# Kernel tuning notes

Measured on AMD Instinct MI355X. Metric: run time of the kernel, lower is better.

## Reference

```python
import jax, jax.numpy as jnp
import numpy as np

# Geometry constants (equidistant flat-detector fan beam)
B, A, D = 16, 1024, 1024      # batch, n_projections, detector bins
H, W = 512, 512               # reconstruction grid
VX = 1.0                      # pixel spacing (mm)
DU = 1.25                     # detector bin spacing (mm)
D_SI = 750.0                  # source-isocenter distance (mm)
D_SD = 1200.0                 # source-detector distance (mm)


def setup_inputs() -> dict:
    key = jax.random.key(0)
    sino = jax.random.normal(key, (B, A, D), dtype=jnp.float32)
    # Ram-Lak ramp filter in FFT ordering (matches torch.fft.fft bin layout)
    filt = jnp.asarray(np.abs(np.fft.fftfreq(D)).astype(np.float32))
    angles = jnp.asarray(np.linspace(0.0, 2.0 * np.pi, A, endpoint=False).astype(np.float32))
    return {"sinogram": sino, "filt": filt, "angles": angles}


def _backproject(fsino, angles):
    # fsino: [B, A, D] filtered sinogram -> image [B, H, W]
    xs = (jnp.arange(W, dtype=jnp.float32) - (W - 1) / 2.0) * VX
    ys = (jnp.arange(H, dtype=jnp.float32) - (H - 1) / 2.0) * VX
    X, Y = jnp.meshgrid(xs, ys, indexing="xy")  # [H, W] world coords (mm)

    def body(acc, inp):
        beta, proj = inp  # beta scalar, proj [B, D]
        c, s = jnp.cos(beta), jnp.sin(beta)
        t = D_SI + X * c + Y * s            # distance from source along central ray [H,W]
        u = D_SD * (-X * s + Y * c) / t     # detector coordinate (mm) [H,W]
        idx = u / DU + (D - 1) / 2.0        # fractional detector index
        i0 = jnp.clip(jnp.floor(idx), 0, D - 2).astype(jnp.int32)
        frac = jnp.clip(idx - i0.astype(jnp.float32), 0.0, 1.0)
        inside = (idx >= 0.0) & (idx <= D - 1.0)
        v0 = jnp.take(proj, i0, axis=1)       # [B, H, W]
        v1 = jnp.take(proj, i0 + 1, axis=1)   # [B, H, W]
        val = v0 * (1.0 - frac) + v1 * frac
        w = (D_SI / t) ** 2                   # fan-beam distance weighting
        acc = acc + jnp.where(inside, val * w, 0.0)
        return acc, None

    acc0 = jnp.zeros((B, H, W), jnp.float32)
    acc, _ = jax.lax.scan(body, acc0, (angles, jnp.swapaxes(fsino, 0, 1)))
    return acc * (jnp.pi / A)  # angular integration step


def reference(sinogram, filt, angles):
    # FFT ramp filtering along detector axis (ortho norm, as in torch code)
    f = jnp.fft.fft(sinogram, axis=-1, norm="ortho")
    f = f * filt
    x = jnp.fft.ifft(f, axis=-1, norm="ortho").real.astype(jnp.float32)
    return _backproject(x, angles)
```

## Files before the change

kernel.cpp:

```cpp
#include <hip/hip_runtime.h>
#include <hip/hip_fp16.h>
#include <math.h>

#define N_B 16
#define N_A 1024
#define N_D 1024
#define N_H 512
#define N_W 512

typedef _Float16 half2t __attribute__((ext_vector_type(2)));
typedef unsigned uint4v __attribute__((ext_vector_type(4)));

__device__ inline half2t h2cast(unsigned u) {
    union { unsigned u; half2t h; } cv; cv.u = u; return cv.h;
}

__device__ inline float fdot2f(half2t a, half2t b, float c) {
#if __has_builtin(__builtin_amdgcn_fdot2)
    return __builtin_amdgcn_fdot2(a, b, c, false);
#else
    asm("v_dot2_f32_f16 %0, %1, %2, %0" : "+v"(c) : "v"(a), "v"(b));
    return c;
#endif
}

__device__ inline half2t pack_h2(float lo, float hi) {
#if __has_builtin(__builtin_amdgcn_cvt_pkrtz)
    auto r = __builtin_amdgcn_cvt_pkrtz(lo, hi);
    union { decltype(r) a; half2t h; } cv; cv.a = r; return cv.h;
#else
    half2t r; r.x = (_Float16)lo; r.y = (_Float16)hi; return r;
#endif
}

__device__ inline unsigned pack_u(float lo, float hi) {
    union { half2t h; unsigned u; } cv; cv.h = pack_h2(lo, hi); return cv.u;
}

__device__ inline float med3f(float a, float lo, float hi) {
#if __has_builtin(__builtin_amdgcn_fmed3f)
    return __builtin_amdgcn_fmed3f(a, lo, hi);
#else
    return fminf(fmaxf(a, lo), hi);
#endif
}

__global__ void fan_setup_kernel(const float* __restrict__ angles,
                                 float* __restrict__ twr,
                                 float* __restrict__ twi,
                                 float2* __restrict__ cs) {
    int t = blockIdx.x * 256 + threadIdx.x;
    if (t < 512) {
        double ang = -2.0 * M_PI * (double)t / 1024.0;
        twr[t] = (float)cos(ang);
        twi[t] = (float)sin(ang);
    }
    if (t < 1024) {
        double b = (double)angles[t];
        cs[t] = make_float2((float)cos(b), (float)sin(b));
    }
}

__global__ __launch_bounds__(256) void fan_fft_filter4_kernel(
    const float* __restrict__ sino, const float* __restrict__ filt,
    const float* __restrict__ twr_g, const float* __restrict__ twi_g,
    uint4* __restrict__ pf4) {
    __shared__ float s_re0[1024], s_im0[1024];
    __shared__ float s_re1[1024], s_im1[1024];
    __shared__ float s_twr[512], s_twi[512];

    const int tid = threadIdx.x;
    const int a = blockIdx.x & (N_A - 1);
    const int g = blockIdx.x >> 10;

    {
        float2 t0 = ((const float2*)twr_g)[tid];
        s_twr[2 * tid] = t0.x; s_twr[2 * tid + 1] = t0.y;
        float2 t1 = ((const float2*)twi_g)[tid];
        s_twi[2 * tid] = t1.x; s_twi[2 * tid + 1] = t1.y;
    }
    {
        const size_t rowstride = (size_t)N_A * N_D;
        const float* rb = sino + (size_t)(4 * g) * rowstride + (size_t)a * N_D;
        ((float4*)s_re0)[tid] = ((const float4*)(rb + 0 * rowstride))[tid];
        ((float4*)s_im0)[tid] = ((const float4*)(rb + 1 * rowstride))[tid];
        ((float4*)s_re1)[tid] = ((const float4*)(rb + 2 * rowstride))[tid];
        ((float4*)s_im1)[tid] = ((const float4*)(rb + 3 * rowstride))[tid];
    }
    __syncthreads();

    for (int L = 9; L >= 0; --L) {
        const int half = 1 << L;
#pragma unroll
        for (int q = 0; q < 4; ++q) {
            float* re = (q < 2) ? s_re0 : s_re1;
            float* im = (q < 2) ? s_im0 : s_im1;
            const int bf = tid + ((q & 1) << 8);
            const int j = bf & (half - 1);
            const int blk = bf >> L;
            const int base = (blk << (L + 1)) + j;
            const int tw = j << (9 - L);
            const float wr = s_twr[tw], wi = s_twi[tw];
            const float ar = re[base], ai = im[base];
            const float br = re[base + half], bi = im[base + half];
            re[base] = ar + br;
            im[base] = ai + bi;
            const float dr = ar - br, di = ai - bi;
            re[base + half] = dr * wr - di * wi;
            im[base + half] = dr * wi + di * wr;
        }
        __syncthreads();
    }

#pragma unroll
    for (int q = 0; q < 4; ++q) {
        const int i = tid + (q << 8);
        const int ri = (int)(__brev((unsigned)i) >> 22);
        const float f = filt[ri];
        s_re0[i] *= f; s_im0[i] *= f;
        s_re1[i] *= f; s_im1[i] *= f;
    }
    __syncthreads();

    for (int L = 0; L <= 9; ++L) {
        const int half = 1 << L;
#pragma unroll
        for (int q = 0; q < 4; ++q) {
            float* re = (q < 2) ? s_re0 : s_re1;
            float* im = (q < 2) ? s_im0 : s_im1;
            const int bf = tid + ((q & 1) << 8);
            const int j = bf & (half - 1);
            const int blk = bf >> L;
            const int base = (blk << (L + 1)) + j;
            const int tw = j << (9 - L);
            const float wr = s_twr[tw], wi = -s_twi[tw];
            const float ar = re[base], ai = im[base];
            const float tr = re[base + half], ti = im[base + half];
            const float br = tr * wr - ti * wi;
            const float bi = tr * wi + ti * wr;
            re[base] = ar + br;
            im[base] = ai + bi;
            re[base + half] = ar - br;
            im[base + half] = ai - bi;
        }
        __syncthreads();
    }

    const float invN = 1.0f / 1024.0f;
    uint4* dst = pf4 + ((size_t)g * N_A + (size_t)a) * N_D;
#pragma unroll
    for (int q = 0; q < 4; ++q) {
        const int n = tid + (q << 8);
        const int n1 = (n < 1023) ? n + 1 : n;
        const float e = (n < 1023) ? 1.0f : 0.0f;
        uint4 v;
        v.x = pack_u(s_re0[n] * invN, s_re0[n1] * invN * e);
        v.y = pack_u(s_im0[n] * invN, s_im0[n1] * invN * e);
        v.z = pack_u(s_re1[n] * invN, s_re1[n1] * invN * e);
        v.w = pack_u(s_im1[n] * invN, s_im1[n1] * invN * e);
        dst[n] = v;
    }
}

#define GEOM(A_, WP0_, WP1_, OFF_)                                            \
    {                                                                         \
        const int a_ = (A_);                                                  \
        const float2 csp = lcs[a_];                                          \
        const float c = csp.x, s = csp.y;                                    \
        const float t = fmaf(x, c, fmaf(y, s, 750.0f));                      \
        const float r = __builtin_amdgcn_rcpf(t);                            \
        const float num = fmaf(y, c, -(x * s));                              \
        const float idx = fmaf(num * r, 960.0f, 511.5f);                     \
        const float idxc = med3f(idx, 0.0f, 1023.0f);                        \
        const float i0f = floorf(idxc);                                      \
        const float frac = idxc - i0f;                                       \
        const float wr_ = 750.0f * r;                                        \
        float wd = wr_ * wr_;                                                \
        wd = (idx == idxc) ? wd : 0.0f;                                      \
        const float w1 = wd * frac;                                          \
        const float w0 = wd - w1;                                            \
        WP0_ = w0; WP1_ = w1;                                                \
        OFF_ = (((unsigned)a_ << 10) + (unsigned)(int)i0f) << 4;             \
    }

#define ISSUE4(V0_, V1_, V2_, V3_, OFF_)                                      \
    asm volatile(                                                             \
        "global_load_dwordx4 %0, %4, %5\n\t"                                  \
        "global_load_dwordx4 %1, %4, %6\n\t"                                  \
        "global_load_dwordx4 %2, %4, %7\n\t"                                  \
        "global_load_dwordx4 %3, %4, %8"                                      \
        : "=&v"(V0_), "=&v"(V1_), "=&v"(V2_), "=&v"(V3_)                      \
        : "v"(OFF_), "s"(g0), "s"(g1), "s"(g2), "s"(g3));

#define VMWAIT(N_)                                                            \
    {                                                                         \
        asm volatile("s_waitcnt vmcnt(" #N_ ")" ::: "memory");                \
        __builtin_amdgcn_sched_barrier(0);                                    \
    }

#define CONSUME1(WP_, V0_, V1_, V2_, V3_)                                     \
    {                                                                         \
        acc[0] = fdot2f(h2cast(V0_[0]), WP_, acc[0]);                         \
        acc[1] = fdot2f(h2cast(V0_[1]), WP_, acc[1]);                         \
        acc[2] = fdot2f(h2cast(V0_[2]), WP_, acc[2]);                         \
        acc[3] = fdot2f(h2cast(V0_[3]), WP_, acc[3]);                         \
        acc[4] = fdot2f(h2cast(V1_[0]), WP_, acc[4]);                         \
        acc[5] = fdot2f(h2cast(V1_[1]), WP_, acc[5]);                         \
        acc[6] = fdot2f(h2cast(V1_[2]), WP_, acc[6]);                         \
        acc[7] = fdot2f(h2cast(V1_[3]), WP_, acc[7]);                         \
        acc[8] = fdot2f(h2cast(V2_[0]), WP_, acc[8]);                         \
        acc[9] = fdot2f(h2cast(V2_[1]), WP_, acc[9]);                         \
        acc[10] = fdot2f(h2cast(V2_[2]), WP_, acc[10]);                       \
        acc[11] = fdot2f(h2cast(V2_[3]), WP_, acc[11]);                       \
        acc[12] = fdot2f(h2cast(V3_[0]), WP_, acc[12]);                       \
        acc[13] = fdot2f(h2cast(V3_[1]), WP_, acc[13]);                       \
        acc[14] = fdot2f(h2cast(V3_[2]), WP_, acc[14]);                       \
        acc[15] = fdot2f(h2cast(V3_[3]), WP_, acc[15]);                       \
    }

#define ISSUE_PAIR(X, AA)                                                     \
    {                                                                         \
        float w0a, w1a, w0b, w1b;                                             \
        unsigned offa, offb;                                                  \
        GEOM((AA), w0a, w1a, offa);                                           \
        GEOM((AA) + 1, w0b, w1b, offb);                                       \
        wp##X##0 = pack_h2(w0a, w1a);                                         \
        wp##X##1 = pack_h2(w0b, w1b);                                         \
        ISSUE4(X##a0, X##a1, X##a2, X##a3, offa);                             \
        ISSUE4(X##b0, X##b1, X##b2, X##b3, offb);                             \
    }

#define CONSUME_PAIR(X)                                                       \
    {                                                                         \
        CONSUME1(wp##X##0, X##a0, X##a1, X##a2, X##a3);                       \
        CONSUME1(wp##X##1, X##b0, X##b1, X##b2, X##b3);                       \
    }

#define BODY(T, S, AA)                                                        \
    {                                                                         \
        ISSUE_PAIR(T, (AA));                                                  \
        VMWAIT(8);                                                            \
        CONSUME_PAIR(S);                                                      \
    }

template <int SPLIT>
__global__ __launch_bounds__(256) void fan_backproject_kernel(
    const uint4* __restrict__ pf4, const float2* __restrict__ cs_g,
    float* __restrict__ dst0, float* __restrict__ dst1) {
    __shared__ float2 lcs[N_A];
    const int tid = threadIdx.x;
#pragma unroll
    for (int q = 0; q < 4; ++q) {
        const int a = tid + (q << 8);
        lcs[a] = cs_g[a];
    }
    __syncthreads();

    const unsigned nwg = gridDim.x;
    const unsigned swz = (blockIdx.x & 7) * (nwg >> 3) + (blockIdx.x >> 3);
    const int part = (SPLIT >= 2) ? (int)(swz >> 10) : 0;
    const int tb = (SPLIT >= 2) ? (int)(swz & 1023) : (int)swz;
    const int ACNT = N_A / SPLIT;
    const int abase = part * ACNT;

    const int tile_x = tb & 31;
    const int tile_y = tb >> 5;
    const int tx = tid & 15;
    const int ty = tid >> 4;
    const int xi = tile_x * 16 + tx;
    const int yi = tile_y * 16 + ty;
    const float x = ((float)xi - 255.5f);
    const float y = ((float)yi - 255.5f);

    const unsigned* g0 = (const unsigned*)pf4;
    const unsigned* g1 = g0 + ((size_t)1 << 22);
    const unsigned* g2 = g0 + ((size_t)2 << 22);
    const unsigned* g3 = g0 + ((size_t)3 << 22);

    float acc[N_B];
#pragma unroll
    for (int b = 0; b < N_B; ++b) acc[b] = 0.0f;

    half2t wpA0, wpA1, wpB0, wpB1;
    uint4v Aa0, Aa1, Aa2, Aa3, Ab0, Ab1, Ab2, Ab3;
    uint4v Ba0, Ba1, Ba2, Ba3, Bb0, Bb1, Bb2, Bb3;

    ISSUE_PAIR(A, abase);
    int aa = abase + 2;
    BODY(B, A, aa);
    aa += 2;
    for (int it = 0; it < (ACNT >> 2) - 1; ++it) {
        BODY(A, B, aa);
        aa += 2;
        BODY(B, A, aa);
        aa += 2;
    }
    VMWAIT(0);
    CONSUME_PAIR(B);

    const float scale = 3.14159265358979323846f / 1024.0f;
    float* dst = (SPLIT >= 2 && part == 1) ? dst1 : dst0;
    const size_t pix = (size_t)yi * N_W + (size_t)xi;
#pragma unroll
    for (int b = 0; b < N_B; ++b) {
        dst[(size_t)b * (N_H * N_W) + pix] = acc[b] * scale;
    }
}

__global__ __launch_bounds__(256) void fan_reduce_kernel(
    const float4* __restrict__ a, const float4* __restrict__ b,
    float4* __restrict__ o) {
    const int i = blockIdx.x * 256 + threadIdx.x;
    const float4 va = a[i], vb = b[i];
    o[i] = make_float4(va.x + vb.x, va.y + vb.y, va.z + vb.z, va.w + vb.w);
}

extern "C" void kernel_launch(void* const* d_in, const int* in_sizes, int n_in,
                              void* d_out, int out_size, void* d_ws, size_t ws_size,
                              hipStream_t stream) {
    const float* sino = (const float*)d_in[0];
    const float* filt = (const float*)d_in[1];
    const float* angles = (const float*)d_in[2];
    float* out = (float*)d_out;

    float* twr = (float*)d_ws;
    float* twi = twr + 512;
    float2* cs = (float2*)(twi + 512);
    char* base = (char*)d_ws;
    uint4* pf4 = (uint4*)(base + 16384);
    const size_t PF_BYTES = (size_t)4 * N_A * N_D * 16;
    float* partial0 = (float*)(base + 16384 + PF_BYTES);
    float* partial1 = partial0 + (size_t)N_B * N_H * N_W;
    const size_t need = 16384 + PF_BYTES + 2 * (size_t)N_B * N_H * N_W * 4;

    fan_setup_kernel<<<4, 256, 0, stream>>>(angles, twr, twi, cs);
    fan_fft_filter4_kernel<<<4 * N_A, 256, 0, stream>>>(sino, filt, twr, twi,
                                                        pf4);
    if (ws_size >= need) {
        fan_backproject_kernel<2><<<(N_H * N_W) / 256 * 2, 256, 0, stream>>>(
            pf4, cs, partial0, partial1);
        fan_reduce_kernel<<<(N_B * N_H * N_W) / 4 / 256, 256, 0, stream>>>(
            (const float4*)partial0, (const float4*)partial1, (float4*)out);
    } else {
        fan_backproject_kernel<1><<<(N_H * N_W) / 256, 256, 0, stream>>>(
            pf4, cs, out, out);
    }
}
```

Measured before the change: 557.3 us.

## Interleave filtered sinogram groups, split angles eight ways, and deepen the load pipeline

The FFT kernel now writes the four batch groups interleaved, so each (angle, detector) sample sits in 64 contiguous bytes. The backprojection fetches it with one base pointer and immediate offsets instead of four separate streams. The angle range is split across eight partial images instead of two, and those are summed by a generalized reduce kernel. The backprojection loop becomes a three-stage, one-angle-per-stage pipeline with a launch-bounds occupancy hint. This trades more parallelism and better load locality for extra partial-image write and read traffic, plus the register limit implied by the occupancy hint.

```diff
diff --git a/kernel.cpp b/kernel.cpp
--- a/kernel.cpp
+++ b/kernel.cpp
@@ -147,7 +147,7 @@
     }
 
     const float invN = 1.0f / 1024.0f;
-    uint4* dst = pf4 + ((size_t)g * N_A + (size_t)a) * N_D;
+    uint4* dst = pf4 + ((size_t)a * 4096 + (size_t)g);
 #pragma unroll
     for (int q = 0; q < 4; ++q) {
         const int n = tid + (q << 8);
@@ -158,39 +158,39 @@
         v.y = pack_u(s_im0[n] * invN, s_im0[n1] * invN * e);
         v.z = pack_u(s_re1[n] * invN, s_re1[n1] * invN * e);
         v.w = pack_u(s_im1[n] * invN, s_im1[n1] * invN * e);
-        dst[n] = v;
-    }
-}
-
-#define GEOM(A_, WP0_, WP1_, OFF_)                                            \
+        dst[(size_t)n * 4] = v;
+    }
+}
+
+#define GEOM(A_, WP_, OFF_)                                                   \
     {                                                                         \
         const int a_ = (A_);                                                  \
-        const float2 csp = lcs[a_];                                          \
-        const float c = csp.x, s = csp.y;                                    \
-        const float t = fmaf(x, c, fmaf(y, s, 750.0f));                      \
-        const float r = __builtin_amdgcn_rcpf(t);                            \
-        const float num = fmaf(y, c, -(x * s));                              \
-        const float idx = fmaf(num * r, 960.0f, 511.5f);                     \
-        const float idxc = med3f(idx, 0.0f, 1023.0f);                        \
-        const float i0f = floorf(idxc);                                      \
-        const float frac = idxc - i0f;                                       \
-        const float wr_ = 750.0f * r;                                        \
-        float wd = wr_ * wr_;                                                \
-        wd = (idx == idxc) ? wd : 0.0f;                                      \
-        const float w1 = wd * frac;                                          \
-        const float w0 = wd - w1;                                            \
-        WP0_ = w0; WP1_ = w1;                                                \
-        OFF_ = (((unsigned)a_ << 10) + (unsigned)(int)i0f) << 4;             \
+        const float2 csp = lcs[a_];                                           \
+        const float c = csp.x, s = csp.y;                                     \
+        const float t = fmaf(x, c, fmaf(y, s, 750.0f));                       \
+        const float r = __builtin_amdgcn_rcpf(t);                             \
+        const float num = fmaf(y, c, -(x * s));                               \
+        const float idx = fmaf(num * r, 960.0f, 511.5f);                      \
+        const float idxc = med3f(idx, 0.0f, 1023.0f);                         \
+        const float i0f = floorf(idxc);                                       \
+        const float frac = idxc - i0f;                                        \
+        const float wr_ = 750.0f * r;                                         \
+        float wd = wr_ * wr_;                                                 \
+        wd = (idx == idxc) ? wd : 0.0f;                                       \
+        const float w1 = wd * frac;                                           \
+        const float w0 = wd - w1;                                             \
+        WP_ = pack_h2(w0, w1);                                                \
+        OFF_ = (((unsigned)a_ << 10) + (unsigned)(int)i0f) << 6;              \
     }
 
 #define ISSUE4(V0_, V1_, V2_, V3_, OFF_)                                      \
     asm volatile(                                                             \
         "global_load_dwordx4 %0, %4, %5\n\t"                                  \
-        "global_load_dwordx4 %1, %4, %6\n\t"                                  \
-        "global_load_dwordx4 %2, %4, %7\n\t"                                  \
-        "global_load_dwordx4 %3, %4, %8"                                      \
+        "global_load_dwordx4 %1, %4, %5 offset:16\n\t"                        \
+        "global_load_dwordx4 %2, %4, %5 offset:32\n\t"                        \
+        "global_load_dwordx4 %3, %4, %5 offset:48"                            \
         : "=&v"(V0_), "=&v"(V1_), "=&v"(V2_), "=&v"(V3_)                      \
-        : "v"(OFF_), "s"(g0), "s"(g1), "s"(g2), "s"(g3));
+        : "v"(OFF_), "s"(gB));
 
 #define VMWAIT(N_)                                                            \
     {                                                                         \
@@ -198,7 +198,7 @@
         __builtin_amdgcn_sched_barrier(0);                                    \
     }
 
-#define CONSUME1(WP_, V0_, V1_, V2_, V3_)                                     \
+#define CONSUME(WP_, V0_, V1_, V2_, V3_)                                      \
     {                                                                         \
         acc[0] = fdot2f(h2cast(V0_[0]), WP_, acc[0]);                         \
         acc[1] = fdot2f(h2cast(V0_[1]), WP_, acc[1]);                         \
@@ -218,35 +218,24 @@
         acc[15] = fdot2f(h2cast(V3_[3]), WP_, acc[15]);                       \
     }
 
-#define ISSUE_PAIR(X, AA)                                                     \
-    {                                                                         \
-        float w0a, w1a, w0b, w1b;                                             \
-        unsigned offa, offb;                                                  \
-        GEOM((AA), w0a, w1a, offa);                                           \
-        GEOM((AA) + 1, w0b, w1b, offb);                                       \
-        wp##X##0 = pack_h2(w0a, w1a);                                         \
-        wp##X##1 = pack_h2(w0b, w1b);                                         \
-        ISSUE4(X##a0, X##a1, X##a2, X##a3, offa);                             \
-        ISSUE4(X##b0, X##b1, X##b2, X##b3, offb);                             \
-    }
-
-#define CONSUME_PAIR(X)                                                       \
-    {                                                                         \
-        CONSUME1(wp##X##0, X##a0, X##a1, X##a2, X##a3);                       \
-        CONSUME1(wp##X##1, X##b0, X##b1, X##b2, X##b3);                       \
+#define ISSUE_ONE(X, AA)                                                      \
+    {                                                                         \
+        unsigned off_;                                                        \
+        GEOM((AA), wp##X, off_);                                              \
+        ISSUE4(X##0, X##1, X##2, X##3, off_);                                 \
     }
 
 #define BODY(T, S, AA)                                                        \
     {                                                                         \
-        ISSUE_PAIR(T, (AA));                                                  \
+        ISSUE_ONE(T, (AA));                                                   \
         VMWAIT(8);                                                            \
-        CONSUME_PAIR(S);                                                      \
+        CONSUME(wp##S, S##0, S##1, S##2, S##3);                               \
     }
 
 template <int SPLIT>
-__global__ __launch_bounds__(256) void fan_backproject_kernel(
+__global__ __launch_bounds__(256, 4) void fan_backproject_kernel(
     const uint4* __restrict__ pf4, const float2* __restrict__ cs_g,
-    float* __restrict__ dst0, float* __restrict__ dst1) {
+    float* __restrict__ dst0) {
     __shared__ float2 lcs[N_A];
     const int tid = threadIdx.x;
 #pragma unroll
@@ -256,10 +245,19 @@
     }
     __syncthreads();
 
-    const unsigned nwg = gridDim.x;
-    const unsigned swz = (blockIdx.x & 7) * (nwg >> 3) + (blockIdx.x >> 3);
-    const int part = (SPLIT >= 2) ? (int)(swz >> 10) : 0;
-    const int tb = (SPLIT >= 2) ? (int)(swz & 1023) : (int)swz;
+    int part, tb;
+    if (SPLIT == 8) {
+        part = blockIdx.x & 7;
+        tb = blockIdx.x >> 3;
+    } else if (SPLIT == 2) {
+        const unsigned nwg = gridDim.x;
+        const unsigned swz = (blockIdx.x & 7) * (nwg >> 3) + (blockIdx.x >> 3);
+        part = (int)(swz >> 10);
+        tb = (int)(swz & 1023);
+    } else {
+        part = 0;
+        tb = blockIdx.x;
+    }
     const int ACNT = N_A / SPLIT;
     const int abase = part * ACNT;
 
@@ -272,34 +270,31 @@
     const float x = ((float)xi - 255.5f);
     const float y = ((float)yi - 255.5f);
 
-    const unsigned* g0 = (const unsigned*)pf4;
-    const unsigned* g1 = g0 + ((size_t)1 << 22);
-    const unsigned* g2 = g0 + ((size_t)2 << 22);
-    const unsigned* g3 = g0 + ((size_t)3 << 22);
+    const unsigned* gB = (const unsigned*)pf4;
 
     float acc[N_B];
 #pragma unroll
     for (int b = 0; b < N_B; ++b) acc[b] = 0.0f;
 
-    half2t wpA0, wpA1, wpB0, wpB1;
-    uint4v Aa0, Aa1, Aa2, Aa3, Ab0, Ab1, Ab2, Ab3;
-    uint4v Ba0, Ba1, Ba2, Ba3, Bb0, Bb1, Bb2, Bb3;
-
-    ISSUE_PAIR(A, abase);
+    half2t wpA, wpB, wpC;
+    uint4v A0, A1, A2, A3, B0, B1, B2, B3, C0, C1, C2, C3;
+
+    ISSUE_ONE(A, abase + 0);
+    ISSUE_ONE(B, abase + 1);
     int aa = abase + 2;
-    BODY(B, A, aa);
-    aa += 2;
-    for (int it = 0; it < (ACNT >> 2) - 1; ++it) {
-        BODY(A, B, aa);
-        aa += 2;
-        BODY(B, A, aa);
-        aa += 2;
-    }
+    for (int it = 0; it < (ACNT - 2) / 3; ++it) {
+        BODY(C, A, aa);
+        BODY(A, B, aa + 1);
+        BODY(B, C, aa + 2);
+        aa += 3;
+    }
+    VMWAIT(4);
+    CONSUME(wpA, A0, A1, A2, A3);
     VMWAIT(0);
-    CONSUME_PAIR(B);
+    CONSUME(wpB, B0, B1, B2, B3);
 
     const float scale = 3.14159265358979323846f / 1024.0f;
-    float* dst = (SPLIT >= 2 && part == 1) ? dst1 : dst0;
+    float* dst = dst0 + (size_t)part * ((size_t)N_B * N_H * N_W);
     const size_t pix = (size_t)yi * N_W + (size_t)xi;
 #pragma unroll
     for (int b = 0; b < N_B; ++b) {
@@ -307,12 +302,18 @@
     }
 }
 
+template <int NS>
 __global__ __launch_bounds__(256) void fan_reduce_kernel(
-    const float4* __restrict__ a, const float4* __restrict__ b,
-    float4* __restrict__ o) {
+    const float4* __restrict__ p, float4* __restrict__ o) {
     const int i = blockIdx.x * 256 + threadIdx.x;
-    const float4 va = a[i], vb = b[i];
-    o[i] = make_float4(va.x + vb.x, va.y + vb.y, va.z + vb.z, va.w + vb.w);
+    const size_t stride = (size_t)N_B * N_H * N_W / 4;
+    float4 v = p[i];
+#pragma unroll
+    for (int k = 1; k < NS; ++k) {
+        const float4 w = p[(size_t)k * stride + i];
+        v.x += w.x; v.y += w.y; v.z += w.z; v.w += w.w;
+    }
+    o[i] = v;
 }
 
 extern "C" void kernel_launch(void* const* d_in, const int* in_sizes, int n_in,
@@ -328,21 +329,26 @@
     float2* cs = (float2*)(twi + 512);
     char* base = (char*)d_ws;
     uint4* pf4 = (uint4*)(base + 16384);
-    const size_t PF_BYTES = (size_t)4 * N_A * N_D * 16;
-    float* partial0 = (float*)(base + 16384 + PF_BYTES);
-    float* partial1 = partial0 + (size_t)N_B * N_H * N_W;
-    const size_t need = 16384 + PF_BYTES + 2 * (size_t)N_B * N_H * N_W * 4;
+    const size_t PF_BYTES = (size_t)N_A * N_D * 64;
+    float* partials = (float*)(base + 16384 + PF_BYTES);
+    const size_t PART = (size_t)N_B * N_H * N_W;
+    const size_t need8 = 16384 + PF_BYTES + 8 * PART * 4;
+    const size_t need2 = 16384 + PF_BYTES + 2 * PART * 4;
 
     fan_setup_kernel<<<4, 256, 0, stream>>>(angles, twr, twi, cs);
     fan_fft_filter4_kernel<<<4 * N_A, 256, 0, stream>>>(sino, filt, twr, twi,
                                                         pf4);
-    if (ws_size >= need) {
-        fan_backproject_kernel<2><<<(N_H * N_W) / 256 * 2, 256, 0, stream>>>(
-            pf4, cs, partial0, partial1);
-        fan_reduce_kernel<<<(N_B * N_H * N_W) / 4 / 256, 256, 0, stream>>>(
-            (const float4*)partial0, (const float4*)partial1, (float4*)out);
+    if (ws_size >= need8) {
+        fan_backproject_kernel<8><<<1024 * 8, 256, 0, stream>>>(pf4, cs,
+                                                                partials);
+        fan_reduce_kernel<8><<<(int)(PART / 4 / 256), 256, 0, stream>>>(
+            (const float4*)partials, (float4*)out);
+    } else if (ws_size >= need2) {
+        fan_backproject_kernel<2><<<1024 * 2, 256, 0, stream>>>(pf4, cs,
+                                                                partials);
+        fan_reduce_kernel<2><<<(int)(PART / 4 / 256), 256, 0, stream>>>(
+            (const float4*)partials, (float4*)out);
     } else {
-        fan_backproject_kernel<1><<<(N_H * N_W) / 256, 256, 0, stream>>>(
-            pf4, cs, out, out);
-    }
-}
+        fan_backproject_kernel<1><<<1024, 256, 0, stream>>>(pf4, cs, out);
+    }
+}
```

Measured after the change: 1.200 ms. 115% more time.
